# Kernel tuning notes

Measured on AMD Instinct MI355X. Metric: run time of the kernel, lower is better.

Reference implementation:

```python
import jax, jax.numpy as jnp
import numpy as np

WINDOW = 128  # window_size from init_kwargs
D = 1024      # input_dim
S = 8192      # seq_len


def setup_inputs() -> dict:
    key = jax.random.key(0)
    k1, k2, k3, k4, k5 = jax.random.split(key, 5)
    bound = 1.0 / np.sqrt(D)
    x = jax.random.normal(k1, (1, S, D), dtype=jnp.float32)
    Wq = jax.random.uniform(k2, (D, D), minval=-bound, maxval=bound, dtype=jnp.float32)
    bq = jax.random.uniform(k3, (D,), minval=-bound, maxval=bound, dtype=jnp.float32)
    Wk = jax.random.uniform(k4, (D, D), minval=-bound, maxval=bound, dtype=jnp.float32)
    bk = jax.random.uniform(k5, (D,), minval=-bound, maxval=bound, dtype=jnp.float32)
    return {"x": x, "Wq": Wq, "bq": bq, "Wk": Wk, "bk": bk}


def reference(x, Wq, bq, Wk, bk):
    # x: [1, S, D]  (original code only works with batch==1)
    xs = x[0]                          # [S, D]
    q = xs @ Wq.T + bq                 # [S, D]
    k = xs @ Wk.T + bk                 # [S, D]
    scores = q @ k.T                   # [S, S] dense, matches original buffer
    t = jnp.arange(S)[:, None]
    s = jnp.arange(S)[None, :]
    # original writes scores only for s in [t-WINDOW, t+WINDOW); elsewhere stays 0
    inwin = (s >= t - WINDOW) & (s < t + WINDOW)
    scores = jnp.where(inwin, scores, 0.0)
    attn = jax.nn.softmax(scores, axis=1)  # softmax INCLUDES the zero entries, as in original
    out = attn @ xs                    # [S, D]
    return out
```

## Files before the change

kernel.cpp:

```cpp
#include <hip/hip_runtime.h>

#define S 8192
#define D 1024
#define WINDOW 128
#define TQ 16
#define UMAX 288
#define BK 32
#define PAD 68
#define BAND 320

typedef __attribute__((ext_vector_type(8))) short short8;
typedef __attribute__((ext_vector_type(4))) float floatx4;
typedef __attribute__((ext_vector_type(4))) unsigned short ushort4v;
typedef unsigned short u16t;

__device__ __forceinline__ float wave_sum(float v) {
  #pragma unroll
  for (int off = 32; off > 0; off >>= 1) v += __shfl_xor(v, off, 64);
  return v;
}
__device__ __forceinline__ float wave_max(float v) {
  #pragma unroll
  for (int off = 32; off > 0; off >>= 1) v = fmaxf(v, __shfl_xor(v, off, 64));
  return v;
}
__device__ __forceinline__ unsigned int f2bf_rn(float f) {
  unsigned int u = __float_as_uint(f);
  return (u + 0x7fffu + ((u >> 16) & 1u)) >> 16;
}


__global__ __launch_bounds__(256) void uv_kernel(
    const float* __restrict__ Wq, const float* __restrict__ Wk,
    const float* __restrict__ bq, const float* __restrict__ bk,
    float* __restrict__ u, float* __restrict__ v, float* __restrict__ cbuf)
{
  const int i = blockIdx.x * 256 + threadIdx.x;
  const int n0 = blockIdx.y * 128;
  float us = 0.f, vs = 0.f;
  for (int n = n0; n < n0 + 128; ++n) {
    us += Wq[(size_t)n * D + i] * bk[n];
    vs += Wk[(size_t)n * D + i] * bq[n];
  }
  atomicAdd(&u[i], us);
  atomicAdd(&v[i], vs);
  if (blockIdx.x == 0 && blockIdx.y == 0) {
    float cs = 0.f;
    for (int n = threadIdx.x; n < D; n += 256) cs += bq[n] * bk[n];
    atomicAdd(cbuf, cs);
  }
}

__global__ __launch_bounds__(256) void prep_kernel(
    const float* __restrict__ x, const float* __restrict__ u,
    const float* __restrict__ v, u16t* __restrict__ xhi, u16t* __restrict__ xlo,
    u16t* __restrict__ xT, float* __restrict__ xsum,
    float* __restrict__ a, float* __restrict__ b)
{
  __shared__ float tile[64][65];
  const int s0 = blockIdx.x * 64;
  const int d0 = blockIdx.y * 64;
  const int t = threadIdx.x;
  #pragma unroll
  for (int p = 0; p < 4; ++p) {
    int r = (t >> 4) + p * 16;
    int c = (t & 15) * 4;
    float4 vv = *(const float4*)(x + (size_t)(s0 + r) * D + d0 + c);
    float f[4] = {vv.x, vv.y, vv.z, vv.w};
    tile[r][c+0] = vv.x; tile[r][c+1] = vv.y; tile[r][c+2] = vv.z; tile[r][c+3] = vv.w;
    ushort4v h, l;
    #pragma unroll
    for (int e = 0; e < 4; ++e) {
      unsigned int hb = f2bf_rn(f[e]);
      float hf = __uint_as_float(hb << 16);
      h[e] = (u16t)hb;
      l[e] = (u16t)f2bf_rn(f[e] - hf);
    }
    size_t idx = (size_t)(s0 + r) * D + d0 + c;
    *(ushort4v*)(xhi + idx) = h;
    *(ushort4v*)(xlo + idx) = l;
  }
  __syncthreads();
  #pragma unroll
  for (int p = 0; p < 4; ++p) {
    int dd = (t >> 4) + p * 16;
    int ss = (t & 15) * 4;
    ushort4v o;
    #pragma unroll
    for (int e = 0; e < 4; ++e) o[e] = (u16t)f2bf_rn(tile[ss + e][dd]);
    *(ushort4v*)(xT + (size_t)(d0 + dd) * S + s0 + ss) = o;
  }
  if (t < 64) {
    float s = 0.f;
    #pragma unroll 8
    for (int r = 0; r < 64; ++r) s += tile[r][t];
    atomicAdd(&xsum[d0 + t], s);
  } else if (t < 128) {
    int r = t - 64;
    float s = 0.f;
    for (int c = 0; c < 64; ++c) s += tile[r][c] * u[d0 + c];
    atomicAdd(&a[s0 + r], s);
  } else if (t < 192) {
    int r = t - 128;
    float s = 0.f;
    for (int c = 0; c < 64; ++c) s += tile[r][c] * v[d0 + c];
    atomicAdd(&b[s0 + r], s);
  }
}

__global__ __launch_bounds__(256) void transposeW_kernel(
    const float* __restrict__ Wq, const float* __restrict__ Wk,
    u16t* __restrict__ wqth, u16t* __restrict__ wqtl,
    u16t* __restrict__ wkth, u16t* __restrict__ wktl)
{
  __shared__ float tile[64][65];
  const float* W = blockIdx.z ? Wk : Wq;
  u16t* oh = blockIdx.z ? wkth : wqth;
  u16t* ol = blockIdx.z ? wktl : wqtl;
  const int n0 = blockIdx.x * 64;
  const int i0 = blockIdx.y * 64;
  const int t = threadIdx.x;
  #pragma unroll
  for (int p = 0; p < 4; ++p) {
    int r = (t >> 4) + p * 16;
    int c = (t & 15) * 4;
    float4 vv = *(const float4*)(W + (size_t)(n0 + r) * D + i0 + c);
    tile[r][c+0] = vv.x; tile[r][c+1] = vv.y; tile[r][c+2] = vv.z; tile[r][c+3] = vv.w;
  }
  __syncthreads();
  #pragma unroll
  for (int p = 0; p < 4; ++p) {
    int ii = (t >> 4) + p * 16;
    int nn = (t & 15) * 4;
    ushort4v h, l;
    #pragma unroll
    for (int e = 0; e < 4; ++e) {
      float f = tile[nn + e][ii];
      unsigned int hb = f2bf_rn(f);
      float hf = __uint_as_float(hb << 16);
      h[e] = (u16t)hb;
      l[e] = (u16t)f2bf_rn(f - hf);
    }
    size_t idx = (size_t)(i0 + ii) * D + n0 + nn;
    *(ushort4v*)(oh + idx) = h;
    *(ushort4v*)(ol + idx) = l;
  }
}

__global__ __launch_bounds__(256) void m_kernel(
    const u16t* __restrict__ wqth, const u16t* __restrict__ wqtl,
    const u16t* __restrict__ wkth, const u16t* __restrict__ wktl,
    u16t* __restrict__ mh, u16t* __restrict__ ml)
{
  __shared__ __align__(16) u16t Mbuf[4][64 * BK];

  const int tid  = threadIdx.x;
  const int lane = tid & 63;
  const int wv   = tid >> 6;
  const int i0   = blockIdx.x * 64;
  const int j0   = blockIdx.y * 64;

  floatx4 acc[2][2] = {};
  const int m0w = (wv & 1) * 32;
  const int n0w = (wv >> 1) * 32;
  const int srow = lane >> 2;
  const int scolw = ((lane & 3) ^ ((lane >> 3) & 3)) * 8;
  const int rs    = (((lane >> 4) ^ ((lane >> 1) & 3)) * 8);

  for (int k0 = 0; k0 < D; k0 += BK) {
    __syncthreads();
    {
      const u16t* src = (wv == 0) ? wqth : (wv == 1) ? wqtl : (wv == 2) ? wkth : wktl;
      const int base  = (wv < 2) ? i0 : j0;
      #pragma unroll
      for (int sg = 0; sg < 4; ++sg) {
        int row = base + sg * 16 + srow;
        size_t g = (size_t)row * D + k0 + scolw;
        __builtin_amdgcn_global_load_lds(
            (const __attribute__((address_space(1))) void*)(src + g),
            (__attribute__((address_space(3))) void*)(&Mbuf[wv][sg * 512]), 16, 0, 0);
      }
    }
    __syncthreads();
    short8 ah[2], al[2], bh[2], bl[2];
    #pragma unroll
    for (int t = 0; t < 2; ++t) {
      int ar = (m0w + t * 16 + (lane & 15)) * BK + rs;
      int br = (n0w + t * 16 + (lane & 15)) * BK + rs;
      ah[t] = *(const short8*)&Mbuf[0][ar];
      al[t] = *(const short8*)&Mbuf[1][ar];
      bh[t] = *(const short8*)&Mbuf[2][br];
      bl[t] = *(const short8*)&Mbuf[3][br];
    }
    #pragma unroll
    for (int mt = 0; mt < 2; ++mt)
      #pragma unroll
      for (int nt = 0; nt < 2; ++nt) {
        acc[mt][nt] = __builtin_amdgcn_mfma_f32_16x16x32_bf16(ah[mt], bh[nt], acc[mt][nt], 0, 0, 0);
        acc[mt][nt] = __builtin_amdgcn_mfma_f32_16x16x32_bf16(ah[mt], bl[nt], acc[mt][nt], 0, 0, 0);
        acc[mt][nt] = __builtin_amdgcn_mfma_f32_16x16x32_bf16(al[mt], bh[nt], acc[mt][nt], 0, 0, 0);
      }
  }
  #pragma unroll
  for (int mt = 0; mt < 2; ++mt)
    #pragma unroll
    for (int nt = 0; nt < 2; ++nt) {
      int j = j0 + n0w + nt * 16 + (lane & 15);
      int i = i0 + m0w + mt * 16 + (lane >> 4) * 4;
      #pragma unroll
      for (int r = 0; r < 4; ++r) {
        float f = acc[mt][nt][r];
        unsigned int hb = f2bf_rn(f);
        float hf = __uint_as_float(hb << 16);
        size_t idx = (size_t)(i + r) * D + j;
        mh[idx] = (u16t)hb;
        ml[idx] = (u16t)f2bf_rn(f - hf);
      }
    }
}

__global__ __launch_bounds__(256) void y_kernel(
    const u16t* __restrict__ xhi, const u16t* __restrict__ xlo,
    const u16t* __restrict__ mhp, const u16t* __restrict__ mlp,
    u16t* __restrict__ yh, u16t* __restrict__ yl)
{
  __shared__ __align__(16) u16t Ah[2 * 128 * BK];
  __shared__ __align__(16) u16t Al[2 * 128 * BK];
  __shared__ __align__(16) u16t Bh[2 * 128 * BK];
  __shared__ __align__(16) u16t Bl[2 * 128 * BK];

  const int tid  = threadIdx.x;
  const int lane = tid & 63;
  const int wv   = tid >> 6;
  const int s0   = blockIdx.x * 128;
  const int i0   = blockIdx.y * 128;

  floatx4 acc[4][4] = {};
  const int m0w  = (wv & 1) * 64;
  const int n0w  = (wv >> 1) * 64;
  const int srow = lane >> 2;
  const int scolw = ((lane & 3) ^ ((lane >> 3) & 3)) * 8;
  const int rs    = (((lane >> 4) ^ ((lane >> 1) & 3)) * 8);

  for (int k0 = 0; k0 < D; k0 += 64) {
    __syncthreads();
    #pragma unroll
    for (int h = 0; h < 2; ++h) {
      #pragma unroll
      for (int sg = 0; sg < 2; ++sg) {
        int seg  = wv * 2 + sg;
        int arow = s0 + seg * 16 + srow;
        int brow = i0 + seg * 16 + srow;
        size_t ga = (size_t)arow * D + k0 + h * 32 + scolw;
        size_t gb = (size_t)brow * D + k0 + h * 32 + scolw;
        int lb = h * 4096 + seg * 512;
        __builtin_amdgcn_global_load_lds(
            (const __attribute__((address_space(1))) void*)(xhi + ga),
            (__attribute__((address_space(3))) void*)(&Ah[lb]), 16, 0, 0);
        __builtin_amdgcn_global_load_lds(
            (const __attribute__((address_space(1))) void*)(xlo + ga),
            (__attribute__((address_space(3))) void*)(&Al[lb]), 16, 0, 0);
        __builtin_amdgcn_global_load_lds(
            (const __attribute__((address_space(1))) void*)(mhp + gb),
            (__attribute__((address_space(3))) void*)(&Bh[lb]), 16, 0, 0);
        __builtin_amdgcn_global_load_lds(
            (const __attribute__((address_space(1))) void*)(mlp + gb),
            (__attribute__((address_space(3))) void*)(&Bl[lb]), 16, 0, 0);
      }
    }
    __syncthreads();
    #pragma unroll
    for (int h = 0; h < 2; ++h) {
      short8 ah[4], al[4], bh[4], bl[4];
      #pragma unroll
      for (int t = 0; t < 4; ++t) {
        int ar = h * 4096 + (m0w + t * 16 + (lane & 15)) * BK + rs;
        int br = h * 4096 + (n0w + t * 16 + (lane & 15)) * BK + rs;
        ah[t] = *(const short8*)&Ah[ar];
        al[t] = *(const short8*)&Al[ar];
        bh[t] = *(const short8*)&Bh[br];
        bl[t] = *(const short8*)&Bl[br];
      }
      #pragma unroll
      for (int mt = 0; mt < 4; ++mt)
        #pragma unroll
        for (int nt = 0; nt < 4; ++nt) {
          acc[mt][nt] = __builtin_amdgcn_mfma_f32_16x16x32_bf16(ah[mt], bh[nt], acc[mt][nt], 0, 0, 0);
          acc[mt][nt] = __builtin_amdgcn_mfma_f32_16x16x32_bf16(ah[mt], bl[nt], acc[mt][nt], 0, 0, 0);
          acc[mt][nt] = __builtin_amdgcn_mfma_f32_16x16x32_bf16(al[mt], bh[nt], acc[mt][nt], 0, 0, 0);
        }
    }
  }
  #pragma unroll
  for (int mt = 0; mt < 4; ++mt)
    #pragma unroll
    for (int nt = 0; nt < 4; ++nt) {
      int i = i0 + n0w + nt * 16 + (lane & 15);
      int s = s0 + m0w + mt * 16 + (lane >> 4) * 4;
      #pragma unroll
      for (int r = 0; r < 4; ++r) {
        float f = acc[mt][nt][r];
        unsigned int hb = f2bf_rn(f);
        float hf = __uint_as_float(hb << 16);
        size_t idx = (size_t)(s + r) * D + i;
        yh[idx] = (u16t)hb;
        yl[idx] = (u16t)f2bf_rn(f - hf);
      }
    }
}

__global__ __launch_bounds__(256) void scores_kernel(
    const u16t* __restrict__ xhi, const u16t* __restrict__ xlo,
    const u16t* __restrict__ yh, const u16t* __restrict__ yl,
    const float* __restrict__ a, const float* __restrict__ b,
    const float* __restrict__ cbuf, float* __restrict__ band)
{
  __shared__ __align__(16) u16t Ah[2 * 64 * BK];
  __shared__ __align__(16) u16t Al[2 * 64 * BK];
  __shared__ __align__(16) u16t Bh[2 * 64 * BK];
  __shared__ __align__(16) u16t Bl[2 * 64 * BK];

  const int tid  = threadIdx.x;
  const int lane = tid & 63;
  const int wv   = tid >> 6;
  const int t0   = blockIdx.x * 64;
  const int jt   = blockIdx.y;
  const int s_base = t0 - 128 + jt * 64;
  const float cval = cbuf[0];

  floatx4 acc[2][2] = {};
  const int m0w  = (wv & 1) * 32;
  const int n0w  = (wv >> 1) * 32;
  const int srow = lane >> 2;
  const int scolw = ((lane & 3) ^ ((lane >> 3) & 3)) * 8;
  const int rs    = (((lane >> 4) ^ ((lane >> 1) & 3)) * 8);

  for (int k0 = 0; k0 < D; k0 += 64) {
    __syncthreads();
    #pragma unroll
    for (int h = 0; h < 2; ++h) {
      int arow = t0 + wv * 16 + srow;
      int brow = s_base + wv * 16 + srow;
      brow = min(max(brow, 0), S - 1);
      size_t ga = (size_t)arow * D + k0 + h * 32 + scolw;
      size_t gb = (size_t)brow * D + k0 + h * 32 + scolw;
      int lb = h * 2048 + wv * 512;
      __builtin_amdgcn_global_load_lds(
          (const __attribute__((address_space(1))) void*)(xhi + ga),
          (__attribute__((address_space(3))) void*)(&Ah[lb]), 16, 0, 0);
      __builtin_amdgcn_global_load_lds(
          (const __attribute__((address_space(1))) void*)(xlo + ga),
          (__attribute__((address_space(3))) void*)(&Al[lb]), 16, 0, 0);
      __builtin_amdgcn_global_load_lds(
          (const __attribute__((address_space(1))) void*)(yh + gb),
          (__attribute__((address_space(3))) void*)(&Bh[lb]), 16, 0, 0);
      __builtin_amdgcn_global_load_lds(
          (const __attribute__((address_space(1))) void*)(yl + gb),
          (__attribute__((address_space(3))) void*)(&Bl[lb]), 16, 0, 0);
    }
    __syncthreads();
    #pragma unroll
    for (int h = 0; h < 2; ++h) {
      short8 ah[2], al[2], bh[2], bl[2];
      #pragma unroll
      for (int t = 0; t < 2; ++t) {
        int ar = h * 2048 + (m0w + t * 16 + (lane & 15)) * BK + rs;
        int br = h * 2048 + (n0w + t * 16 + (lane & 15)) * BK + rs;
        ah[t] = *(const short8*)&Ah[ar];
        al[t] = *(const short8*)&Al[ar];
        bh[t] = *(const short8*)&Bh[br];
        bl[t] = *(const short8*)&Bl[br];
      }
      #pragma unroll
      for (int mt = 0; mt < 2; ++mt)
        #pragma unroll
        for (int nt = 0; nt < 2; ++nt) {
          acc[mt][nt] = __builtin_amdgcn_mfma_f32_16x16x32_bf16(ah[mt], bh[nt], acc[mt][nt], 0, 0, 0);
          acc[mt][nt] = __builtin_amdgcn_mfma_f32_16x16x32_bf16(ah[mt], bl[nt], acc[mt][nt], 0, 0, 0);
          acc[mt][nt] = __builtin_amdgcn_mfma_f32_16x16x32_bf16(al[mt], bh[nt], acc[mt][nt], 0, 0, 0);
        }
    }
  }
  #pragma unroll
  for (int mt = 0; mt < 2; ++mt)
    #pragma unroll
    for (int nt = 0; nt < 2; ++nt) {
      int n_loc = n0w + nt * 16 + (lane & 15);
      int s = s_base + n_loc;
      float bv = (s >= 0 && s < S) ? b[s] : 0.f;
      #pragma unroll
      for (int r = 0; r < 4; ++r) {
        int m_loc = m0w + mt * 16 + (lane >> 4) * 4 + r;
        int t = t0 + m_loc;
        bool inwin = (s >= t - WINDOW) && (s < t + WINDOW) && (s >= 0) && (s < S);
        float sv = inwin ? (acc[mt][nt][r] + a[t] + bv + cval) : 0.f;
        band[(size_t)t * BAND + jt * 64 + n_loc] = sv;
      }
    }
}

__global__ __launch_bounds__(256) void softmax_kernel(
    const float* __restrict__ band, u16t* __restrict__ Pb, float* __restrict__ e0d)
{
  const int lane = threadIdx.x & 63;
  const int w    = threadIdx.x >> 6;
  const int t    = blockIdx.x * 4 + w;
  const float* row = band + (size_t)t * BAND;
  float v[5];
  float mx = 0.f;
  #pragma unroll
  for (int i = 0; i < 5; ++i) {
    v[i] = row[i * 64 + lane];
    mx = fmaxf(mx, v[i]);
  }
  mx = wave_max(mx);
  float e0 = __expf(-mx);
  float ss = 0.f;
  #pragma unroll
  for (int i = 0; i < 5; ++i) {
    v[i] = __expf(v[i] - mx);
    ss += v[i];
  }
  ss = wave_sum(ss);
  float dinv = 1.f / (ss + (float)(S - BAND) * e0);
  #pragma unroll
  for (int i = 0; i < 5; ++i)
    Pb[(size_t)t * BAND + i * 64 + lane] = (u16t)f2bf_rn((v[i] - e0) * dinv);
  if (lane == 0) e0d[t] = e0 * dinv;
}

__global__ __launch_bounds__(256) void pv_kernel(
    const u16t* __restrict__ Pb, const u16t* __restrict__ xT,
    const float* __restrict__ e0d, const float* __restrict__ xsum,
    float* __restrict__ out)
{
  __shared__ __align__(16) u16t Ab[2 * 64 * BK];
  __shared__ __align__(16) u16t Bb[2 * 128 * BK];

  const int tid  = threadIdx.x;
  const int lane = tid & 63;
  const int wv   = tid >> 6;
  const int t0   = blockIdx.x * 64;
  const int d0   = blockIdx.y * 128;
  const int origin = t0 - 128;

  floatx4 acc[2][4] = {};
  const int m0w  = (wv & 1) * 32;
  const int n0w  = (wv >> 1) * 64;
  const int srow = lane >> 2;
  const int scolw = ((lane & 3) ^ ((lane >> 3) & 3)) * 8;
  const int rs    = (((lane >> 4) ^ ((lane >> 1) & 3)) * 8);

  for (int k0 = 0; k0 < BAND; k0 += 64) {
    __syncthreads();
    #pragma unroll
    for (int h = 0; h < 2; ++h) {
      {
        int arow = t0 + wv * 16 + srow;
        size_t ga = (size_t)arow * BAND + k0 + h * 32 + scolw;
        int lb = h * 2048 + wv * 512;
        __builtin_amdgcn_global_load_lds(
            (const __attribute__((address_space(1))) void*)(Pb + ga),
            (__attribute__((address_space(3))) void*)(&Ab[lb]), 16, 0, 0);
      }
      #pragma unroll
      for (int sg = 0; sg < 2; ++sg) {
        int seg  = wv * 2 + sg;
        int brow = d0 + seg * 16 + srow;
        int s_g  = origin + k0 + h * 32 + scolw;
        s_g = min(max(s_g, 0), S - 8);
        size_t gb = (size_t)brow * S + s_g;
        int lb = h * 4096 + seg * 512;
        __builtin_amdgcn_global_load_lds(
            (const __attribute__((address_space(1))) void*)(xT + gb),
            (__attribute__((address_space(3))) void*)(&Bb[lb]), 16, 0, 0);
      }
    }
    __syncthreads();
    #pragma unroll
    for (int h = 0; h < 2; ++h) {
      short8 af[2], bf[4];
      #pragma unroll
      for (int t = 0; t < 2; ++t) {
        int ar = h * 2048 + (m0w + t * 16 + (lane & 15)) * BK + rs;
        af[t] = *(const short8*)&Ab[ar];
      }
      #pragma unroll
      for (int t = 0; t < 4; ++t) {
        int br = h * 4096 + (n0w + t * 16 + (lane & 15)) * BK + rs;
        bf[t] = *(const short8*)&Bb[br];
      }
      #pragma unroll
      for (int mt = 0; mt < 2; ++mt)
        #pragma unroll
        for (int nt = 0; nt < 4; ++nt)
          acc[mt][nt] = __builtin_amdgcn_mfma_f32_16x16x32_bf16(af[mt], bf[nt], acc[mt][nt], 0, 0, 0);
    }
  }
  #pragma unroll
  for (int mt = 0; mt < 2; ++mt)
    #pragma unroll
    for (int nt = 0; nt < 4; ++nt) {
      int n_g = d0 + n0w + nt * 16 + (lane & 15);
      float xs = xsum[n_g];
      #pragma unroll
      for (int r = 0; r < 4; ++r) {
        int m_g = t0 + m0w + mt * 16 + (lane >> 4) * 4 + r;
        out[(size_t)m_g * D + n_g] = acc[mt][nt][r] + e0d[m_g] * xs;
      }
    }
}

__global__ __launch_bounds__(256) void proj_kernel(
    const float* __restrict__ x, const float* __restrict__ Wq,
    const float* __restrict__ bqv, const float* __restrict__ Wk,
    const float* __restrict__ bkv, float* __restrict__ qout,
    float* __restrict__ kout)
{
  __shared__ __align__(16) float xs[BK][PAD];
  __shared__ __align__(16) float wqs[BK][PAD];
  __shared__ __align__(16) float wks[BK][PAD];
  const int tid = threadIdx.x;
  const int tx = tid & 15, ty = tid >> 4;
  const int t0 = blockIdx.x * 64, i0 = blockIdx.y * 64;
  float accq[4][4] = {}, acck[4][4] = {};
  const int lrow0 = tid >> 3, lc4 = (tid & 7) * 4;
  for (int k0 = 0; k0 < D; k0 += BK) {
    __syncthreads();
    #pragma unroll
    for (int p = 0; p < 2; ++p) {
      int row = lrow0 + p * 32;
      float4 a = *(const float4*)(x  + (size_t)(t0 + row) * D + k0 + lc4);
      float4 b = *(const float4*)(Wq + (size_t)(i0 + row) * D + k0 + lc4);
      float4 c = *(const float4*)(Wk + (size_t)(i0 + row) * D + k0 + lc4);
      xs [lc4+0][row]=a.x; xs [lc4+1][row]=a.y; xs [lc4+2][row]=a.z; xs [lc4+3][row]=a.w;
      wqs[lc4+0][row]=b.x; wqs[lc4+1][row]=b.y; wqs[lc4+2][row]=b.z; wqs[lc4+3][row]=b.w;
      wks[lc4+0][row]=c.x; wks[lc4+1][row]=c.y; wks[lc4+2][row]=c.z; wks[lc4+3][row]=c.w;
    }
    __syncthreads();
    #pragma unroll
    for (int kk = 0; kk < BK; ++kk) {
      float4 av = *(const float4*)&xs [kk][ty*4];
      float4 bv = *(const float4*)&wqs[kk][tx*4];
      float4 cv = *(const float4*)&wks[kk][tx*4];
      float a[4] = {av.x, av.y, av.z, av.w};
      float b[4] = {bv.x, bv.y, bv.z, bv.w};
      float c[4] = {cv.x, cv.y, cv.z, cv.w};
      #pragma unroll
      for (int r = 0; r < 4; ++r)
        #pragma unroll
        for (int cc = 0; cc < 4; ++cc) {
          accq[r][cc] = fmaf(a[r], b[cc], accq[r][cc]);
          acck[r][cc] = fmaf(a[r], c[cc], acck[r][cc]);
        }
    }
  }
  float4 bq4 = *(const float4*)(bqv + i0 + tx*4);
  float4 bk4 = *(const float4*)(bkv + i0 + tx*4);
  #pragma unroll
  for (int r = 0; r < 4; ++r) {
    int trow = t0 + ty*4 + r;
    float4 oq = { accq[r][0]+bq4.x, accq[r][1]+bq4.y, accq[r][2]+bq4.z, accq[r][3]+bq4.w };
    float4 ok = { acck[r][0]+bk4.x, acck[r][1]+bk4.y, acck[r][2]+bk4.z, acck[r][3]+bk4.w };
    *(float4*)(qout + (size_t)trow * D + i0 + tx*4) = oq;
    *(float4*)(kout + (size_t)trow * D + i0 + tx*4) = ok;
  }
}

__global__ __launch_bounds__(256) void colsum_kernel(const float* __restrict__ x,
                                                     float* __restrict__ xsum)
{
  int d = blockIdx.x * 256 + threadIdx.x;
  int tbase = blockIdx.y * 256;
  float s = 0.f;
  for (int t = 0; t < 256; ++t) s += x[(size_t)(tbase + t) * D + d];
  atomicAdd(&xsum[d], s);
}

__global__ __launch_bounds__(256) void attn_kernel(
    const float* __restrict__ x, const float* __restrict__ q,
    const float* __restrict__ kmat, const float* __restrict__ xsum,
    float* __restrict__ out)
{
  __shared__ __align__(16) float scl[TQ][UMAX];
  __shared__ float e0s[TQ], dinv[TQ];
  const int tid = threadIdx.x, lane = tid & 63, wv = tid >> 6;
  const int t0 = blockIdx.x * TQ;
  const int lo_u = max(0, t0 - WINDOW);
  const int hi_u = min(S, t0 + TQ - 1 + WINDOW);
  const int ucnt = hi_u - lo_u;
  for (int i = tid; i < TQ * UMAX; i += 256) (&scl[0][0])[i] = 0.f;
  __syncthreads();
  {
    const int tiB = wv * 4;
    float4 qf[4][4];
    #pragma unroll
    for (int g = 0; g < 4; ++g) {
      int t = t0 + tiB + g;
      #pragma unroll
      for (int j = 0; j < 4; ++j)
        qf[g][j] = *(const float4*)(q + (size_t)t * D + lane*4 + j*256);
    }
    const int wlo = max(0, t0 + tiB - WINDOW);
    const int whi = min(S, t0 + tiB + 3 + WINDOW);
    for (int s = wlo; s < whi; ++s) {
      float4 kf[4];
      #pragma unroll
      for (int j = 0; j < 4; ++j)
        kf[j] = *(const float4*)(kmat + (size_t)s * D + lane*4 + j*256);
      float acc[4];
      #pragma unroll
      for (int g = 0; g < 4; ++g) {
        float v = 0.f;
        #pragma unroll
        for (int j = 0; j < 4; ++j) {
          v = fmaf(qf[g][j].x, kf[j].x, v);
          v = fmaf(qf[g][j].y, kf[j].y, v);
          v = fmaf(qf[g][j].z, kf[j].z, v);
          v = fmaf(qf[g][j].w, kf[j].w, v);
        }
        acc[g] = v;
      }
      #pragma unroll
      for (int g = 0; g < 4; ++g) {
        float tot = wave_sum(acc[g]);
        int t = t0 + tiB + g;
        if (lane == 0 && s >= t - WINDOW && s < t + WINDOW)
          scl[tiB + g][s - lo_u] = tot;
      }
    }
  }
  __syncthreads();
  #pragma unroll
  for (int g = 0; g < 4; ++g) {
    int ti = wv * 4 + g;
    int t = t0 + ti;
    int lo = max(0, t - WINDOW), hi = min(S, t + WINDOW);
    int cnt = hi - lo, off = lo - lo_u;
    float m = 0.f;
    for (int i = lane; i < cnt; i += 64) m = fmaxf(m, scl[ti][off + i]);
    m = wave_max(m);
    float e0 = __expf(-m);
    float ssum = 0.f;
    for (int i = lane; i < cnt; i += 64) {
      float e = __expf(scl[ti][off + i] - m);
      ssum += e;
      scl[ti][off + i] = e - e0;
    }
    ssum = wave_sum(ssum);
    if (lane == 0) {
      dinv[ti] = 1.f / (ssum + (float)(S - cnt) * e0);
      e0s[ti] = e0;
    }
  }
  __syncthreads();
  {
    const int c4 = tid * 4;
    float4 acc[TQ];
    #pragma unroll
    for (int ti = 0; ti < TQ; ++ti) acc[ti] = make_float4(0.f, 0.f, 0.f, 0.f);
    for (int su = 0; su < ucnt; su += 4) {
      float4 xr[4];
      #pragma unroll
      for (int u = 0; u < 4; ++u)
        xr[u] = *(const float4*)(x + (size_t)(lo_u + su + u) * D + c4);
      #pragma unroll
      for (int ti = 0; ti < TQ; ++ti) {
        float4 w4 = *(const float4*)&scl[ti][su];
        float wvv[4] = {w4.x, w4.y, w4.z, w4.w};
        #pragma unroll
        for (int u = 0; u < 4; ++u) {
          acc[ti].x = fmaf(wvv[u], xr[u].x, acc[ti].x);
          acc[ti].y = fmaf(wvv[u], xr[u].y, acc[ti].y);
          acc[ti].z = fmaf(wvv[u], xr[u].z, acc[ti].z);
          acc[ti].w = fmaf(wvv[u], xr[u].w, acc[ti].w);
        }
      }
    }
    float4 xsv = *(const float4*)(xsum + c4);
    #pragma unroll
    for (int ti = 0; ti < TQ; ++ti) {
      float e0 = e0s[ti], di = dinv[ti];
      float4 o;
      o.x = (acc[ti].x + e0 * xsv.x) * di;
      o.y = (acc[ti].y + e0 * xsv.y) * di;
      o.z = (acc[ti].z + e0 * xsv.z) * di;
      o.w = (acc[ti].w + e0 * xsv.w) * di;
      *(float4*)(out + (size_t)(t0 + ti) * D + c4) = o;
    }
  }
}

extern "C" void kernel_launch(void* const* d_in, const int* in_sizes, int n_in,
                              void* d_out, int out_size, void* d_ws, size_t ws_size,
                              hipStream_t stream) {
  const float* x  = (const float*)d_in[0];
  const float* Wq = (const float*)d_in[1];
  const float* bq = (const float*)d_in[2];
  const float* Wk = (const float*)d_in[3];
  const float* bk = (const float*)d_in[4];
  float* outp = (float*)d_out;

  const size_t SD = (size_t)S * D;
  const size_t DD = (size_t)D * D;

  float* xsum = (float*)d_ws;
  float* u    = xsum + D;
  float* v    = u + D;
  float* a    = v + D;
  float* b    = a + S;
  float* cbuf = b + S;
  size_t zero_bytes = (size_t)(3 * D + 2 * S + 16) * sizeof(float);

  u16t* xhi  = (u16t*)(cbuf + 16);
  u16t* xlo  = xhi + SD;
  u16t* xT   = xlo + SD;
  u16t* wqth = xT + SD;
  u16t* wqtl = wqth + DD;
  u16t* wkth = wqtl + DD;
  u16t* wktl = wkth + DD;
  u16t* mh   = wktl + DD;
  u16t* ml   = mh + DD;
  u16t* yh   = ml + DD;
  u16t* yl   = yh + SD;
  float* band = (float*)(yl + SD);
  u16t*  Pb   = (u16t*)(band + (size_t)S * BAND);
  float* e0d  = (float*)(Pb + (size_t)S * BAND);
  size_t needed = (size_t)((char*)(e0d + S) - (char*)d_ws);

  if (ws_size >= needed) {
    (void)hipMemsetAsync(d_ws, 0, zero_bytes, stream);
    uv_kernel<<<dim3(D / 256, 8), 256, 0, stream>>>(Wq, Wk, bq, bk, u, v, cbuf);
    prep_kernel<<<dim3(S / 64, D / 64), 256, 0, stream>>>(x, u, v, xhi, xlo, xT, xsum, a, b);
    transposeW_kernel<<<dim3(D / 64, D / 64, 2), 256, 0, stream>>>(Wq, Wk, wqth, wqtl, wkth, wktl);
    m_kernel<<<dim3(D / 64, D / 64), 256, 0, stream>>>(wqth, wqtl, wkth, wktl, mh, ml);
    y_kernel<<<dim3(S / 128, D / 128), 256, 0, stream>>>(xhi, xlo, mh, ml, yh, yl);
    scores_kernel<<<dim3(S / 64, 5), 256, 0, stream>>>(xhi, xlo, yh, yl, a, b, cbuf, band);
    softmax_kernel<<<S / 4, 256, 0, stream>>>(band, Pb, e0d);
    pv_kernel<<<dim3(S / 64, D / 128), 256, 0, stream>>>(Pb, xT, e0d, xsum, outp);
  } else {
    float* xs2  = (float*)d_ws;
    float* q    = xs2 + D;
    float* kbuf = q + SD;
    (void)hipMemsetAsync(xs2, 0, D * sizeof(float), stream);
    colsum_kernel<<<dim3(D / 256, S / 256), 256, 0, stream>>>(x, xs2);
    proj_kernel<<<dim3(S / 64, D / 64), 256, 0, stream>>>(x, Wq, bq, Wk, bk, q, kbuf);
    attn_kernel<<<S / TQ, 256, 0, stream>>>(x, q, kbuf, xs2, outp);
  }
}
```

Before: 264.6 us.

## Rewrite y_kernel with 256x128 tiles, triple-buffered LDS and interleaved prefetch

The y_kernel GEMM (x·M in split-bf16) moves from 128x128 tiles with 256 threads and a load-then-compute loop to 256x128 tiles with 512 threads. It uses a three-stage LDS ring and issues global-to-LDS prefetches two k-steps ahead, spread across the per-mt MFMA groups, with s_setprio raising priority around the MFMA bursts. The goal is to hide global load latency behind matrix-core work and to raise reuse per block. In exchange it uses more LDS, adds many explicit barriers and relies on manual vmcnt waits, which is fragile. A GLDS macro also replaces repeated load-to-LDS calls elsewhere.

```diff
diff --git a/kernel.cpp b/kernel.cpp
--- a/kernel.cpp
+++ b/kernel.cpp
@@ -9,6 +9,11 @@
 #define PAD 68
 #define BAND 320
 
+#define YBM 256
+#define YBN 128
+#define YBK 32
+#define YNT (D / YBK)
+
 typedef __attribute__((ext_vector_type(8))) short short8;
 typedef __attribute__((ext_vector_type(4))) float floatx4;
 typedef __attribute__((ext_vector_type(4))) unsigned short ushort4v;
@@ -28,6 +33,10 @@
   unsigned int u = __float_as_uint(f);
   return (u + 0x7fffu + ((u >> 16) & 1u)) >> 16;
 }
+
+#define GLDS(gp, lp) __builtin_amdgcn_global_load_lds( \
+    (const __attribute__((address_space(1))) void*)(gp), \
+    (__attribute__((address_space(3))) void*)(lp), 16, 0, 0)
 
 
 __global__ __launch_bounds__(256) void uv_kernel(
@@ -176,9 +185,7 @@
       for (int sg = 0; sg < 4; ++sg) {
         int row = base + sg * 16 + srow;
         size_t g = (size_t)row * D + k0 + scolw;
-        __builtin_amdgcn_global_load_lds(
-            (const __attribute__((address_space(1))) void*)(src + g),
-            (__attribute__((address_space(3))) void*)(&Mbuf[wv][sg * 512]), 16, 0, 0);
+        GLDS(src + g, &Mbuf[wv][sg * 512]);
       }
     }
     __syncthreads();
@@ -219,84 +226,158 @@
     }
 }
 
-__global__ __launch_bounds__(256) void y_kernel(
+__global__ __launch_bounds__(512) void y_kernel(
     const u16t* __restrict__ xhi, const u16t* __restrict__ xlo,
     const u16t* __restrict__ mhp, const u16t* __restrict__ mlp,
     u16t* __restrict__ yh, u16t* __restrict__ yl)
 {
-  __shared__ __align__(16) u16t Ah[2 * 128 * BK];
-  __shared__ __align__(16) u16t Al[2 * 128 * BK];
-  __shared__ __align__(16) u16t Bh[2 * 128 * BK];
-  __shared__ __align__(16) u16t Bl[2 * 128 * BK];
+  __shared__ __align__(16) u16t Ah[3][YBM * YBK];
+  __shared__ __align__(16) u16t Al[3][YBM * YBK];
+  __shared__ __align__(16) u16t Bh[3][YBN * YBK];
+  __shared__ __align__(16) u16t Bl[3][YBN * YBK];
 
   const int tid  = threadIdx.x;
   const int lane = tid & 63;
   const int wv   = tid >> 6;
-  const int s0   = blockIdx.x * 128;
-  const int i0   = blockIdx.y * 128;
+  const int wm   = wv >> 1;
+  const int wn   = wv & 1;
+  const int s0   = blockIdx.x * YBM;
+  const int i0   = blockIdx.y * YBN;
+
+  const int strow = tid >> 2;
+  const int gchnk = ((tid & 3) ^ ((tid >> 3) & 3)) * 8;
+  const int lslot = (tid & 3) * 8;
+  const int rs = (((lane >> 4) ^ ((lane >> 1) & 3)) * 8);
+  const int fr = lane & 15;
 
   floatx4 acc[4][4] = {};
-  const int m0w  = (wv & 1) * 64;
-  const int n0w  = (wv >> 1) * 64;
-  const int srow = lane >> 2;
-  const int scolw = ((lane & 3) ^ ((lane >> 3) & 3)) * 8;
-  const int rs    = (((lane >> 4) ^ ((lane >> 1) & 3)) * 8);
-
-  for (int k0 = 0; k0 < D; k0 += 64) {
-    __syncthreads();
-    #pragma unroll
-    for (int h = 0; h < 2; ++h) {
-      #pragma unroll
-      for (int sg = 0; sg < 2; ++sg) {
-        int seg  = wv * 2 + sg;
-        int arow = s0 + seg * 16 + srow;
-        int brow = i0 + seg * 16 + srow;
-        size_t ga = (size_t)arow * D + k0 + h * 32 + scolw;
-        size_t gb = (size_t)brow * D + k0 + h * 32 + scolw;
-        int lb = h * 4096 + seg * 512;
-        __builtin_amdgcn_global_load_lds(
-            (const __attribute__((address_space(1))) void*)(xhi + ga),
-            (__attribute__((address_space(3))) void*)(&Ah[lb]), 16, 0, 0);
-        __builtin_amdgcn_global_load_lds(
-            (const __attribute__((address_space(1))) void*)(xlo + ga),
-            (__attribute__((address_space(3))) void*)(&Al[lb]), 16, 0, 0);
-        __builtin_amdgcn_global_load_lds(
-            (const __attribute__((address_space(1))) void*)(mhp + gb),
-            (__attribute__((address_space(3))) void*)(&Bh[lb]), 16, 0, 0);
-        __builtin_amdgcn_global_load_lds(
-            (const __attribute__((address_space(1))) void*)(mlp + gb),
-            (__attribute__((address_space(3))) void*)(&Bl[lb]), 16, 0, 0);
-      }
-    }
-    __syncthreads();
-    #pragma unroll
-    for (int h = 0; h < 2; ++h) {
-      short8 ah[4], al[4], bh[4], bl[4];
-      #pragma unroll
-      for (int t = 0; t < 4; ++t) {
-        int ar = h * 4096 + (m0w + t * 16 + (lane & 15)) * BK + rs;
-        int br = h * 4096 + (n0w + t * 16 + (lane & 15)) * BK + rs;
-        ah[t] = *(const short8*)&Ah[ar];
-        al[t] = *(const short8*)&Al[ar];
-        bh[t] = *(const short8*)&Bh[br];
-        bl[t] = *(const short8*)&Bl[br];
-      }
-      #pragma unroll
-      for (int mt = 0; mt < 4; ++mt)
-        #pragma unroll
-        for (int nt = 0; nt < 4; ++nt) {
-          acc[mt][nt] = __builtin_amdgcn_mfma_f32_16x16x32_bf16(ah[mt], bh[nt], acc[mt][nt], 0, 0, 0);
-          acc[mt][nt] = __builtin_amdgcn_mfma_f32_16x16x32_bf16(ah[mt], bl[nt], acc[mt][nt], 0, 0, 0);
-          acc[mt][nt] = __builtin_amdgcn_mfma_f32_16x16x32_bf16(al[mt], bh[nt], acc[mt][nt], 0, 0, 0);
-        }
-    }
-  }
+
+  auto STAGE_AH = [&](int kt, int b) {
+    GLDS(xhi + (size_t)(s0 + strow) * D + kt * YBK + gchnk,
+         &Ah[b][strow * YBK + lslot]);
+    GLDS(xhi + (size_t)(s0 + strow + 128) * D + kt * YBK + gchnk,
+         &Ah[b][(strow + 128) * YBK + lslot]);
+  };
+  auto STAGE_AL = [&](int kt, int b) {
+    GLDS(xlo + (size_t)(s0 + strow) * D + kt * YBK + gchnk,
+         &Al[b][strow * YBK + lslot]);
+    GLDS(xlo + (size_t)(s0 + strow + 128) * D + kt * YBK + gchnk,
+         &Al[b][(strow + 128) * YBK + lslot]);
+  };
+  auto STAGE_B = [&](int kt, int b) {
+    GLDS(mhp + (size_t)(i0 + strow) * D + kt * YBK + gchnk,
+         &Bh[b][strow * YBK + lslot]);
+    GLDS(mlp + (size_t)(i0 + strow) * D + kt * YBK + gchnk,
+         &Bl[b][strow * YBK + lslot]);
+  };
+
+  STAGE_AH(0, 0); STAGE_AL(0, 0); STAGE_B(0, 0);
+  STAGE_AH(1, 1); STAGE_AL(1, 1); STAGE_B(1, 1);
+  asm volatile("s_waitcnt vmcnt(6)" ::: "memory");
+  __builtin_amdgcn_s_barrier();
+
+  for (int t = 0; t < YNT; ++t) {
+    const int cur = t % 3;
+    const int nxt = (t + 2) % 3;
+    const bool pf = (t + 2 < YNT);
+    const u16t* pAh = Ah[cur];
+    const u16t* pAl = Al[cur];
+    const u16t* pBh = Bh[cur];
+    const u16t* pBl = Bl[cur];
+
+    short8 bh[4], bl[4];
+    #pragma unroll
+    for (int nt = 0; nt < 4; ++nt) {
+      int br = (wn * 64 + nt * 16 + fr) * YBK + rs;
+      bh[nt] = *(const short8*)&pBh[br];
+      bl[nt] = *(const short8*)&pBl[br];
+    }
+
+    {
+      int ar = (wm * 64 + 0 * 16 + fr) * YBK + rs;
+      short8 ah = *(const short8*)&pAh[ar];
+      short8 al = *(const short8*)&pAl[ar];
+      if (pf) STAGE_AH(t + 2, nxt);
+      __builtin_amdgcn_s_barrier();
+      __builtin_amdgcn_s_setprio(1);
+      #pragma unroll
+      for (int nt = 0; nt < 4; ++nt)
+        acc[0][nt] = __builtin_amdgcn_mfma_f32_16x16x32_bf16(ah, bh[nt], acc[0][nt], 0, 0, 0);
+      #pragma unroll
+      for (int nt = 0; nt < 4; ++nt)
+        acc[0][nt] = __builtin_amdgcn_mfma_f32_16x16x32_bf16(ah, bl[nt], acc[0][nt], 0, 0, 0);
+      #pragma unroll
+      for (int nt = 0; nt < 4; ++nt)
+        acc[0][nt] = __builtin_amdgcn_mfma_f32_16x16x32_bf16(al, bh[nt], acc[0][nt], 0, 0, 0);
+      __builtin_amdgcn_s_setprio(0);
+      __builtin_amdgcn_s_barrier();
+    }
+    {
+      int ar = (wm * 64 + 1 * 16 + fr) * YBK + rs;
+      short8 ah = *(const short8*)&pAh[ar];
+      short8 al = *(const short8*)&pAl[ar];
+      if (pf) STAGE_AL(t + 2, nxt);
+      __builtin_amdgcn_s_barrier();
+      __builtin_amdgcn_s_setprio(1);
+      #pragma unroll
+      for (int nt = 0; nt < 4; ++nt)
+        acc[1][nt] = __builtin_amdgcn_mfma_f32_16x16x32_bf16(ah, bh[nt], acc[1][nt], 0, 0, 0);
+      #pragma unroll
+      for (int nt = 0; nt < 4; ++nt)
+        acc[1][nt] = __builtin_amdgcn_mfma_f32_16x16x32_bf16(ah, bl[nt], acc[1][nt], 0, 0, 0);
+      #pragma unroll
+      for (int nt = 0; nt < 4; ++nt)
+        acc[1][nt] = __builtin_amdgcn_mfma_f32_16x16x32_bf16(al, bh[nt], acc[1][nt], 0, 0, 0);
+      __builtin_amdgcn_s_setprio(0);
+      __builtin_amdgcn_s_barrier();
+    }
+    {
+      int ar = (wm * 64 + 2 * 16 + fr) * YBK + rs;
+      short8 ah = *(const short8*)&pAh[ar];
+      short8 al = *(const short8*)&pAl[ar];
+      if (pf) STAGE_B(t + 2, nxt);
+      __builtin_amdgcn_s_barrier();
+      __builtin_amdgcn_s_setprio(1);
+      #pragma unroll
+      for (int nt = 0; nt < 4; ++nt)
+        acc[2][nt] = __builtin_amdgcn_mfma_f32_16x16x32_bf16(ah, bh[nt], acc[2][nt], 0, 0, 0);
+      #pragma unroll
+      for (int nt = 0; nt < 4; ++nt)
+        acc[2][nt] = __builtin_amdgcn_mfma_f32_16x16x32_bf16(ah, bl[nt], acc[2][nt], 0, 0, 0);
+      #pragma unroll
+      for (int nt = 0; nt < 4; ++nt)
+        acc[2][nt] = __builtin_amdgcn_mfma_f32_16x16x32_bf16(al, bh[nt], acc[2][nt], 0, 0, 0);
+      __builtin_amdgcn_s_setprio(0);
+      __builtin_amdgcn_s_barrier();
+    }
+    {
+      int ar = (wm * 64 + 3 * 16 + fr) * YBK + rs;
+      short8 ah = *(const short8*)&pAh[ar];
+      short8 al = *(const short8*)&pAl[ar];
+      __builtin_amdgcn_s_barrier();
+      __builtin_amdgcn_s_setprio(1);
+      #pragma unroll
+      for (int nt = 0; nt < 4; ++nt)
+        acc[3][nt] = __builtin_amdgcn_mfma_f32_16x16x32_bf16(ah, bh[nt], acc[3][nt], 0, 0, 0);
+      #pragma unroll
+      for (int nt = 0; nt < 4; ++nt)
+        acc[3][nt] = __builtin_amdgcn_mfma_f32_16x16x32_bf16(ah, bl[nt], acc[3][nt], 0, 0, 0);
+      #pragma unroll
+      for (int nt = 0; nt < 4; ++nt)
+        acc[3][nt] = __builtin_amdgcn_mfma_f32_16x16x32_bf16(al, bh[nt], acc[3][nt], 0, 0, 0);
+      __builtin_amdgcn_s_setprio(0);
+      if (t == YNT - 2)      asm volatile("s_waitcnt vmcnt(0)" ::: "memory");
+      else if (t < YNT - 2)  asm volatile("s_waitcnt vmcnt(6)" ::: "memory");
+      __builtin_amdgcn_s_barrier();
+    }
+  }
+
   #pragma unroll
   for (int mt = 0; mt < 4; ++mt)
     #pragma unroll
     for (int nt = 0; nt < 4; ++nt) {
-      int i = i0 + n0w + nt * 16 + (lane & 15);
-      int s = s0 + m0w + mt * 16 + (lane >> 4) * 4;
+      int i = i0 + wn * 64 + nt * 16 + fr;
+      int s = s0 + wm * 64 + mt * 16 + (lane >> 4) * 4;
       #pragma unroll
       for (int r = 0; r < 4; ++r) {
         float f = acc[mt][nt][r];
@@ -345,18 +426,10 @@
       size_t ga = (size_t)arow * D + k0 + h * 32 + scolw;
       size_t gb = (size_t)brow * D + k0 + h * 32 + scolw;
       int lb = h * 2048 + wv * 512;
-      __builtin_amdgcn_global_load_lds(
-          (const __attribute__((address_space(1))) void*)(xhi + ga),
-          (__attribute__((address_space(3))) void*)(&Ah[lb]), 16, 0, 0);
-      __builtin_amdgcn_global_load_lds(
-          (const __attribute__((address_space(1))) void*)(xlo + ga),
-          (__attribute__((address_space(3))) void*)(&Al[lb]), 16, 0, 0);
-      __builtin_amdgcn_global_load_lds(
-          (const __attribute__((address_space(1))) void*)(yh + gb),
-          (__attribute__((address_space(3))) void*)(&Bh[lb]), 16, 0, 0);
-      __builtin_amdgcn_global_load_lds(
-          (const __attribute__((address_space(1))) void*)(yl + gb),
-          (__attribute__((address_space(3))) void*)(&Bl[lb]), 16, 0, 0);
+      GLDS(xhi + ga, &Ah[lb]);
+      GLDS(xlo + ga, &Al[lb]);
+      GLDS(yh + gb, &Bh[lb]);
+      GLDS(yl + gb, &Bl[lb]);
     }
     __syncthreads();
     #pragma unroll
@@ -459,9 +532,7 @@
         int arow = t0 + wv * 16 + srow;
         size_t ga = (size_t)arow * BAND + k0 + h * 32 + scolw;
         int lb = h * 2048 + wv * 512;
-        __builtin_amdgcn_global_load_lds(
-            (const __attribute__((address_space(1))) void*)(Pb + ga),
-            (__attribute__((address_space(3))) void*)(&Ab[lb]), 16, 0, 0);
+        GLDS(Pb + ga, &Ab[lb]);
       }
       #pragma unroll
       for (int sg = 0; sg < 2; ++sg) {
@@ -471,9 +542,7 @@
         s_g = min(max(s_g, 0), S - 8);
         size_t gb = (size_t)brow * S + s_g;
         int lb = h * 4096 + seg * 512;
-        __builtin_amdgcn_global_load_lds(
-            (const __attribute__((address_space(1))) void*)(xT + gb),
-            (__attribute__((address_space(3))) void*)(&Bb[lb]), 16, 0, 0);
+        GLDS(xT + gb, &Bb[lb]);
       }
     }
     __syncthreads();
@@ -734,7 +803,7 @@
     prep_kernel<<<dim3(S / 64, D / 64), 256, 0, stream>>>(x, u, v, xhi, xlo, xT, xsum, a, b);
     transposeW_kernel<<<dim3(D / 64, D / 64, 2), 256, 0, stream>>>(Wq, Wk, wqth, wqtl, wkth, wktl);
     m_kernel<<<dim3(D / 64, D / 64), 256, 0, stream>>>(wqth, wqtl, wkth, wktl, mh, ml);
-    y_kernel<<<dim3(S / 128, D / 128), 256, 0, stream>>>(xhi, xlo, mh, ml, yh, yl);
+    y_kernel<<<dim3(S / YBM, D / YBN), 512, 0, stream>>>(xhi, xlo, mh, ml, yh, yl);
     scores_kernel<<<dim3(S / 64, 5), 256, 0, stream>>>(xhi, xlo, yh, yl, a, b, cbuf, band);
     softmax_kernel<<<S / 4, 256, 0, stream>>>(band, Pb, e0d);
     pv_kernel<<<dim3(S / 64, D / 128), 256, 0, stream>>>(Pb, xT, e0d, xsum, outp);
```

Result: no change. 268.1 us (+1.3%).
